# Kernel tuning notes

Measured on AMD Instinct MI355X. Metric: run time of the kernel, lower is better.

Reference implementation:

```python
import jax, jax.numpy as jnp
import numpy as np

B, S, H, D = 4, 2048, 12, 64
HID = H * D  # 768
EPS = 1e-5


def _layer_norm(h, w, b):
    mu = jnp.mean(h, axis=-1, keepdims=True)
    var = jnp.mean((h - mu) ** 2, axis=-1, keepdims=True)
    return w * (h - mu) / jnp.sqrt(var + EPS) + b


def setup_inputs() -> dict:
    key = jax.random.key(0)
    ks = jax.random.split(key, 12)
    sc = 1.0 / np.sqrt(HID)
    inp = {
        "x": jax.random.normal(ks[0], (B, S, HID), jnp.float32),
        "ln1_w": jnp.ones((HID,), jnp.float32),
        "ln1_b": jnp.zeros((HID,), jnp.float32),
        "Wq": jax.random.normal(ks[1], (HID, HID), jnp.float32) * sc,
        "bq": jnp.zeros((HID,), jnp.float32),
        "Wk": jax.random.normal(ks[2], (HID, HID), jnp.float32) * sc,
        "bk": jnp.zeros((HID,), jnp.float32),
        "Wv": jax.random.normal(ks[3], (HID, HID), jnp.float32) * sc,
        "bv": jnp.zeros((HID,), jnp.float32),
        "Wo": jax.random.normal(ks[4], (HID, HID), jnp.float32) * sc,
        "bo": jnp.zeros((HID,), jnp.float32),
        "ln2_w": jnp.ones((HID,), jnp.float32),
        "ln2_b": jnp.zeros((HID,), jnp.float32),
        "W1": jax.random.normal(ks[5], (HID, 4 * HID), jnp.float32) * sc,
        "b1": jnp.zeros((4 * HID,), jnp.float32),
        "W2": jax.random.normal(ks[6], (4 * HID, HID), jnp.float32) * (1.0 / np.sqrt(4 * HID)),
        "b2": jnp.zeros((HID,), jnp.float32),
    }
    return inp


def _split_heads(t):
    # (B, S, H*D) -> (B, H, S, D)
    b, s, _ = t.shape
    return t.reshape(b, s, H, -1).transpose(0, 2, 1, 3)


def _merge_heads(t):
    # (B, H, S, D) -> (B, S, H*D)
    b, h, s, d = t.shape
    return t.transpose(0, 2, 1, 3).reshape(b, s, h * d)


def _attention(h, Wq, bq, Wk, bk, Wv, bv, Wo, bo):
    q = _split_heads(h @ Wq + bq)  # (B,H,S,D)
    k = _split_heads(h @ Wk + bk)
    v = _split_heads(h @ Wv + bv)
    scores = jnp.einsum("bhqd,bhkd->bhqk", q, k) / jnp.sqrt(jnp.asarray(D, h.dtype))
    causal = jnp.tril(jnp.ones((q.shape[2], q.shape[2]), bool))  # (S,S)
    scores = jnp.where(causal, scores, jnp.finfo(scores.dtype).min)
    w = jax.nn.softmax(scores, axis=-1)
    out = jnp.einsum("bhqk,bhkd->bhqd", w, v)
    return _merge_heads(out) @ Wo + bo


def reference(x, ln1_w, ln1_b, Wq, bq, Wk, bk, Wv, bv, Wo, bo, ln2_w, ln2_b, W1, b1, W2, b2):
    # Pre-LN transformer block: x + attn(LN(x)); then x + MLP(LN(x))
    a = _attention(_layer_norm(x, ln1_w, ln1_b), Wq, bq, Wk, bk, Wv, bv, Wo, bo)
    x = x + a
    h = _layer_norm(x, ln2_w, ln2_b)
    m = jax.nn.gelu(h @ W1 + b1, approximate=False) @ W2 + b2
    return x + m
```

## Files before the change

kernel.cpp:

```cpp
#include <hip/hip_runtime.h>
#include <cmath>
#include <stdint.h>

typedef unsigned short u16;
typedef __attribute__((ext_vector_type(8))) short short8;
typedef __attribute__((ext_vector_type(4))) float f32x4;
typedef __attribute__((ext_vector_type(4))) unsigned int u32x4;

#define HID 768
#define FF  3072
#define SEQ 2048
#define NHEAD 12
#define NROWS 8192

__device__ __forceinline__ float bf2f(u16 u){ return __uint_as_float(((unsigned)u)<<16); }
__device__ __forceinline__ u16 f2bf(float f){
  unsigned x = __float_as_uint(f);
  x += 0x7fffu + ((x>>16)&1u);
  return (u16)(x>>16);
}
__device__ __forceinline__ unsigned pack2(float a, float b){
  return (unsigned)f2bf(a) | ((unsigned)f2bf(b) << 16);
}
__device__ __forceinline__ void gload16(const void* g, void* l){
  __builtin_amdgcn_global_load_lds((const __attribute__((address_space(1))) unsigned*)g,
                                   (__attribute__((address_space(3))) unsigned*)l, 16, 0, 0);
}

__global__ __launch_bounds__(256) void wconv(const float* __restrict__ in,
                                             u16* __restrict__ out, int K, int N)
{
  __shared__ float t[32][33];
  const int bk = blockIdx.x*32, bn = blockIdx.y*32;
  const int tn = threadIdx.x & 31, tk = threadIdx.x >> 5;
  #pragma unroll
  for (int j=0;j<4;++j)
    t[tk+8*j][tn] = in[(size_t)(bk+tk+8*j)*N + bn + tn];
  __syncthreads();
  #pragma unroll
  for (int j=0;j<4;++j)
    out[(size_t)(bn+tk+8*j)*K + bk + tn] = f2bf(t[tn][tk+8*j]);
}

__global__ __launch_bounds__(256) void tconv(const u16* __restrict__ in,
                                             u16* __restrict__ out, int K, int N)
{
  __shared__ u16 t[32][34];
  const int bk = blockIdx.x*32, bn = blockIdx.y*32;
  const int tn = threadIdx.x & 31, tk = threadIdx.x >> 5;
  #pragma unroll
  for (int j=0;j<4;++j)
    t[tk+8*j][tn] = in[(size_t)(bk+tk+8*j)*N + bn + tn];
  __syncthreads();
  #pragma unroll
  for (int j=0;j<4;++j)
    out[(size_t)(bn+tk+8*j)*K + bk + tn] = t[tn][tk+8*j];
}

__global__ __launch_bounds__(256) void ln_k(const float* __restrict__ in,
    const float* __restrict__ gw, const float* __restrict__ gb,
    u16* __restrict__ out)
{
  const int row = blockIdx.x*4 + (threadIdx.x>>6);
  const int l = threadIdx.x & 63;
  const float* p = in + (size_t)row*HID;
  float4 v[3];
  float s=0.f, ss=0.f;
  #pragma unroll
  for (int j=0;j<3;++j){
    v[j] = *(const float4*)(p + j*256 + l*4);
    s  += v[j].x + v[j].y + v[j].z + v[j].w;
    ss += v[j].x*v[j].x + v[j].y*v[j].y + v[j].z*v[j].z + v[j].w*v[j].w;
  }
  #pragma unroll
  for (int m=1;m<64;m<<=1){
    s  += __shfl_xor(s,  m, 64);
    ss += __shfl_xor(ss, m, 64);
  }
  const float mu = s * (1.f/768.f);
  const float rstd = rsqrtf(ss*(1.f/768.f) - mu*mu + 1e-5f);
  #pragma unroll
  for (int j=0;j<3;++j){
    const float4 wv = *(const float4*)(gw + j*256 + l*4);
    const float4 bv = *(const float4*)(gb + j*256 + l*4);
    ushort4 o;
    o.x = f2bf((v[j].x-mu)*rstd*wv.x + bv.x);
    o.y = f2bf((v[j].y-mu)*rstd*wv.y + bv.y);
    o.z = f2bf((v[j].z-mu)*rstd*wv.z + bv.z);
    o.w = f2bf((v[j].w-mu)*rstd*wv.w + bv.w);
    *(ushort4*)(out + (size_t)row*HID + j*256 + l*4) = o;
  }
}

template<int MODE>
__global__ __launch_bounds__(256) void gemm_bt(const u16* __restrict__ A,
    const u16* __restrict__ Bt, const float* __restrict__ bias0,
    const float* __restrict__ bias1, const float* __restrict__ bias2,
    const float* __restrict__ res, void* __restrict__ outp,
    int N, int K, long wstride, long ostride)
{
  __shared__ __align__(16) u16 sA[2][128*32];
  __shared__ __align__(16) u16 sB[2][128*32];
  const int tid = threadIdx.x, l = tid&63, w = tid>>6;
  const int wr = w>>1, wc = w&1, hi = l>>4, lo = l&15;
  const int bm = blockIdx.x*128, bn = blockIdx.y*128;
  const int z = blockIdx.z;
  const u16* Bz = Bt + (size_t)z * (size_t)wstride;
  const float* bias = (z==0) ? bias0 : ((z==1)? bias1 : bias2);

  const u16* Arow = A  + (size_t)bm*K;
  const u16* Brow = Bz + (size_t)bn*K;

  const f32x4 zv = {0.f,0.f,0.f,0.f};
  f32x4 acc[4][4];
  #pragma unroll
  for (int i=0;i<4;++i)
    #pragma unroll
    for (int j=0;j<4;++j) acc[i][j] = zv;

  const int r0_ = tid>>2, off_ = (tid&3)*8;
  const int r1_ = r0_ + 64;

  {
    gload16(Arow + (size_t)r0_*K + off_, (char*)sA[0] + tid*16);
    gload16(Brow + (size_t)r0_*K + off_, (char*)sB[0] + tid*16);
    gload16(Arow + (size_t)r1_*K + off_, (char*)sA[0] + (tid+256)*16);
    gload16(Brow + (size_t)r1_*K + off_, (char*)sB[0] + (tid+256)*16);
  }
  __syncthreads();

  const int NT = K >> 5;
  int cur = 0;
  for (int t=0; t<NT; ++t){
    if (t+1 < NT){
      const int kt = (t+1) << 5;
      gload16(Arow + (size_t)r0_*K + kt + off_, (char*)sA[cur^1] + tid*16);
      gload16(Brow + (size_t)r0_*K + kt + off_, (char*)sB[cur^1] + tid*16);
      gload16(Arow + (size_t)r1_*K + kt + off_, (char*)sA[cur^1] + (tid+256)*16);
      gload16(Brow + (size_t)r1_*K + kt + off_, (char*)sB[cur^1] + (tid+256)*16);
    }
    short8 af[4], bfv[4];
    #pragma unroll
    for (int i=0;i<4;++i){
      af[i]  = *(const short8*)(sA[cur] + (wr*64 + i*16 + lo)*32 + hi*8);
      bfv[i] = *(const short8*)(sB[cur] + (wc*64 + i*16 + lo)*32 + hi*8);
    }
    #pragma unroll
    for (int mi=0;mi<4;++mi)
      #pragma unroll
      for (int ni=0;ni<4;++ni)
        acc[mi][ni] = __builtin_amdgcn_mfma_f32_16x16x32_bf16(af[mi], bfv[ni], acc[mi][ni], 0,0,0);
    __syncthreads();
    cur ^= 1;
  }

  #pragma unroll
  for (int mi=0;mi<4;++mi)
    #pragma unroll
    for (int ni=0;ni<4;++ni){
      const int r0 = bm + wr*64 + mi*16 + 4*hi;
      const int cc = bn + wc*64 + ni*16 + lo;
      const float bv = bias[cc];
      #pragma unroll
      for (int g=0; g<4; ++g){
        const size_t idx = (size_t)(r0+g)*N + cc;
        float v = acc[mi][ni][g] + bv;
        if (MODE == 0){
          ((u16*)outp + (size_t)z*(size_t)ostride)[idx] = f2bf(v);
        } else if (MODE == 1){
          ((float*)outp)[idx] = res[idx] + v;
        } else {
          float u = v*(0.7978845608f + 0.0356774081f*v*v);
          float e = __expf(2.f*u);
          float th = 1.f - 2.f/(1.f + e);
          ((u16*)outp)[idx] = f2bf(0.5f*v*(1.f + th));
        }
      }
    }
}

__global__ __launch_bounds__(256, 4) void attn_k(const u16* __restrict__ Qm,
                                                 const u16* __restrict__ Km,
                                                 const u16* __restrict__ Vt,
                                                 u16* __restrict__ Om)
{
  __shared__ __align__(16) u16 sK [64*64];
  __shared__ __align__(16) u16 sVT[64*64];
  const int tid = threadIdx.x, l = tid & 63, w = tid >> 6;
  const int hi = l >> 4, lo = l & 15;
  const int idx = blockIdx.x;
  const int qb = 31 - (idx / 48);
  const int bh = idx % 48;
  const int b = bh / NHEAD, h = bh - (bh / NHEAD) * NHEAD;
  const size_t rb = (size_t)b * SEQ;
  const int qw = qb*64 + w*16;

  short8 qf[2];
  #pragma unroll
  for (int ks=0; ks<2; ++ks){
    short8 t = *(const short8*)(Qm + (rb + qw + lo)*HID + h*64 + ks*32 + hi*8);
    #pragma unroll
    for (int i=0;i<8;++i) t[i] = (short)f2bf(bf2f((u16)t[i]) * 0.125f);
    qf[ks] = t;
  }

  const f32x4 zv = {0.f,0.f,0.f,0.f};
  f32x4 oa[4] = {zv, zv, zv, zv};
  float m = -INFINITY, lsum = 0.f;
  const int srcA = (((2*hi)  & 3) << 4) | lo;
  const int srcB = (((2*hi+1)& 3) << 4) | lo;

  for (int t=0; t<=qb; ++t){
    const int kv0 = t*64;
    __syncthreads();
    #pragma unroll
    for (int j=0;j<2;++j){
      int c = tid + 256*j;
      int row = c >> 3;
      int d0 = ((c&7) ^ (row&7))*8;
      gload16(Km + (rb + kv0 + row)*HID + h*64 + d0, (char*)sK + c*16);
    }
    #pragma unroll
    for (int j=0;j<2;++j){
      int c = tid + 256*j;
      int row = c >> 3;
      int k0 = ((c&7) ^ (row&7))*8;
      gload16(Vt + (size_t)(h*64 + row)*NROWS + rb + kv0 + k0, (char*)sVT + c*16);
    }
    __syncthreads();

    f32x4 sc[4] = {zv, zv, zv, zv};
    #pragma unroll
    for (int ks=0;ks<2;++ks){
      #pragma unroll
      for (int ni=0;ni<4;++ni){
        short8 kf = *(const short8*)(sK + (ni*16 + lo)*64 + ((ks*32 + hi*8) ^ ((lo&7)*8)));
        sc[ni] = __builtin_amdgcn_mfma_f32_16x16x32_bf16(kf, qf[ks], sc[ni], 0,0,0);
      }
    }

    if (t == qb){
      #pragma unroll
      for (int ni=0;ni<4;++ni)
        #pragma unroll
        for (int g=0; g<4; ++g){
          int kg = kv0 + ni*16 + 4*hi + g;
          if (kg > qw + lo) sc[ni][g] = -INFINITY;
        }
    }

    float pm = sc[0][0];
    #pragma unroll
    for (int ni=0;ni<4;++ni)
      #pragma unroll
      for (int g=0; g<4; ++g) pm = fmaxf(pm, sc[ni][g]);
    pm = fmaxf(pm, __shfl_xor(pm, 16, 64));
    pm = fmaxf(pm, __shfl_xor(pm, 32, 64));
    const float mnew = fmaxf(m, pm);
    const float alpha = __expf(m - mnew);
    float ps = 0.f;
    #pragma unroll
    for (int ni=0;ni<4;++ni)
      #pragma unroll
      for (int g=0; g<4; ++g){
        float e = __expf(sc[ni][g] - mnew);
        sc[ni][g] = e;
        ps += e;
      }
    ps += __shfl_xor(ps, 16, 64);
    ps += __shfl_xor(ps, 32, 64);
    lsum = lsum*alpha + ps;
    m = mnew;
    #pragma unroll
    for (int nd=0;nd<4;++nd){
      oa[nd][0]*=alpha; oa[nd][1]*=alpha; oa[nd][2]*=alpha; oa[nd][3]*=alpha;
    }

    #pragma unroll
    for (int ks=0;ks<2;++ks){
      unsigned pkA0 = pack2(sc[2*ks  ][0], sc[2*ks  ][1]);
      unsigned pkA1 = pack2(sc[2*ks  ][2], sc[2*ks  ][3]);
      unsigned pkB0 = pack2(sc[2*ks+1][0], sc[2*ks+1][1]);
      unsigned pkB1 = pack2(sc[2*ks+1][2], sc[2*ks+1][3]);
      unsigned a0 = (unsigned)__shfl((int)pkA0, srcA, 64);
      unsigned b0 = (unsigned)__shfl((int)pkB0, srcA, 64);
      unsigned a1 = (unsigned)__shfl((int)pkA1, srcA, 64);
      unsigned b1 = (unsigned)__shfl((int)pkB1, srcA, 64);
      unsigned a2 = (unsigned)__shfl((int)pkA0, srcB, 64);
      unsigned b2 = (unsigned)__shfl((int)pkB0, srcB, 64);
      unsigned a3 = (unsigned)__shfl((int)pkA1, srcB, 64);
      unsigned b3 = (unsigned)__shfl((int)pkB1, srcB, 64);
      union { u32x4 u; short8 s; } pf;
      pf.u = (u32x4){ (hi<2)?a0:b0, (hi<2)?a1:b1, (hi<2)?a2:b2, (hi<2)?a3:b3 };

      #pragma unroll
      for (int nd=0;nd<4;++nd){
        short8 vf = *(const short8*)(sVT + (nd*16 + lo)*64 + ((ks*32 + hi*8) ^ ((lo&7)*8)));
        oa[nd] = __builtin_amdgcn_mfma_f32_16x16x32_bf16(vf, pf.s, oa[nd], 0,0,0);
      }
    }
  }

  const float inv = 1.f / lsum;
  #pragma unroll
  for (int nd=0;nd<4;++nd){
    ushort4 o;
    o.x = f2bf(oa[nd][0]*inv);
    o.y = f2bf(oa[nd][1]*inv);
    o.z = f2bf(oa[nd][2]*inv);
    o.w = f2bf(oa[nd][3]*inv);
    *(ushort4*)(Om + (rb + qw + lo)*HID + h*64 + nd*16 + 4*hi) = o;
  }
}

extern "C" void kernel_launch(void* const* d_in, const int* in_sizes, int n_in,
                              void* d_out, int out_size, void* d_ws, size_t ws_size,
                              hipStream_t stream)
{
  const float* x    = (const float*)d_in[0];
  const float* ln1w = (const float*)d_in[1];
  const float* ln1b = (const float*)d_in[2];
  const float* Wq   = (const float*)d_in[3];
  const float* bq   = (const float*)d_in[4];
  const float* Wk   = (const float*)d_in[5];
  const float* bk   = (const float*)d_in[6];
  const float* Wv   = (const float*)d_in[7];
  const float* bv   = (const float*)d_in[8];
  const float* Wo   = (const float*)d_in[9];
  const float* bo   = (const float*)d_in[10];
  const float* ln2w = (const float*)d_in[11];
  const float* ln2b = (const float*)d_in[12];
  const float* W1   = (const float*)d_in[13];
  const float* b1   = (const float*)d_in[14];
  const float* W2   = (const float*)d_in[15];
  const float* b2   = (const float*)d_in[16];

  u16* wq_t = (u16*)d_ws;
  u16* wk_t = wq_t + 589824;
  u16* wv_t = wk_t + 589824;
  u16* wo_t = wv_t + 589824;
  u16* w1_t = wo_t + 589824;
  u16* w2_t = w1_t + 2359296;
  u16* hbf  = w2_t + 2359296;
  u16* qb_  = hbf + 6291456;
  u16* kb_  = qb_ + 6291456;
  u16* vb_  = kb_ + 6291456;
  u16* atb  = vb_ + 6291456;
  u16* ub   = qb_;
  float* x2 = (float*)(atb + 6291456);

  const size_t need = 102236160ull;
  if (ws_size < need) return;

  dim3 blk(256);
  wconv<<<dim3(24,24), blk, 0, stream>>>(Wq, wq_t, 768, 768);
  wconv<<<dim3(24,24), blk, 0, stream>>>(Wk, wk_t, 768, 768);
  wconv<<<dim3(24,24), blk, 0, stream>>>(Wv, wv_t, 768, 768);
  wconv<<<dim3(24,24), blk, 0, stream>>>(Wo, wo_t, 768, 768);
  wconv<<<dim3(24,96), blk, 0, stream>>>(W1, w1_t, 768, 3072);
  wconv<<<dim3(96,24), blk, 0, stream>>>(W2, w2_t, 3072, 768);

  ln_k<<<2048, blk, 0, stream>>>(x, ln1w, ln1b, hbf);

  gemm_bt<0><<<dim3(64,6,3), blk, 0, stream>>>(hbf, wq_t, bq, bk, bv,
      nullptr, (void*)qb_, 768, 768, 589824L, 6291456L);
  tconv<<<dim3(256,24), blk, 0, stream>>>(vb_, hbf, 8192, 768);

  attn_k<<<dim3(1536), blk, 0, stream>>>(qb_, kb_, hbf, atb);

  gemm_bt<1><<<dim3(64,6,1), blk, 0, stream>>>(atb, wo_t, bo, bo, bo,
      x, (void*)x2, 768, 768, 0L, 0L);

  ln_k<<<2048, blk, 0, stream>>>(x2, ln2w, ln2b, hbf);

  gemm_bt<2><<<dim3(64,24,1), blk, 0, stream>>>(hbf, w1_t, b1, b1, b1,
      nullptr, (void*)ub, 3072, 768, 0L, 0L);

  gemm_bt<1><<<dim3(64,6,1), blk, 0, stream>>>(ub, w2_t, b2, b2, b2,
      x2, d_out, 768, 3072, 0L, 0L);
}
```

Baseline: 384.0 us.

## Narrow GEMM N-tiles, use exp2 softmax with lazy rescale and packed bf16 convert

The GEMM is templated on the N tile width. The QKV, out-projection and W2 GEMMs now use 64-wide tiles, doubling block count on the 768-wide outputs to fill more compute units. Attention folds log2(e) into the Q scale so it can use hardware exp2, and skips the rescaling of the accumulator and running sum unless the row max grows by more than 10. It also replaces manual bf16 rounding with the v_cvt_pk_bf16_f32 instruction. The tradeoffs are less data reuse per GEMM tile and slightly different rounding and overflow headroom in softmax.

Measured after the change: 397.4 us. +3.5%, slower.

```diff
diff --git a/kernel.cpp b/kernel.cpp
--- a/kernel.cpp
+++ b/kernel.cpp
@@ -19,8 +19,10 @@
   x += 0x7fffu + ((x>>16)&1u);
   return (u16)(x>>16);
 }
-__device__ __forceinline__ unsigned pack2(float a, float b){
-  return (unsigned)f2bf(a) | ((unsigned)f2bf(b) << 16);
+__device__ __forceinline__ unsigned cvtpk(float a, float b){
+  unsigned r;
+  asm("v_cvt_pk_bf16_f32 %0, %1, %2" : "=v"(r) : "v"(a), "v"(b));
+  return r;
 }
 __device__ __forceinline__ void gload16(const void* g, void* l){
   __builtin_amdgcn_global_load_lds((const __attribute__((address_space(1))) unsigned*)g,
@@ -92,18 +94,19 @@
   }
 }
 
-template<int MODE>
+template<int MODE, int BN>
 __global__ __launch_bounds__(256) void gemm_bt(const u16* __restrict__ A,
     const u16* __restrict__ Bt, const float* __restrict__ bias0,
     const float* __restrict__ bias1, const float* __restrict__ bias2,
     const float* __restrict__ res, void* __restrict__ outp,
     int N, int K, long wstride, long ostride)
 {
+  constexpr int NI = BN/32;
   __shared__ __align__(16) u16 sA[2][128*32];
-  __shared__ __align__(16) u16 sB[2][128*32];
+  __shared__ __align__(16) u16 sB[2][BN*32];
   const int tid = threadIdx.x, l = tid&63, w = tid>>6;
   const int wr = w>>1, wc = w&1, hi = l>>4, lo = l&15;
-  const int bm = blockIdx.x*128, bn = blockIdx.y*128;
+  const int bm = blockIdx.x*128, bn = blockIdx.y*BN;
   const int z = blockIdx.z;
   const u16* Bz = Bt + (size_t)z * (size_t)wstride;
   const float* bias = (z==0) ? bias0 : ((z==1)? bias1 : bias2);
@@ -112,21 +115,20 @@
   const u16* Brow = Bz + (size_t)bn*K;
 
   const f32x4 zv = {0.f,0.f,0.f,0.f};
-  f32x4 acc[4][4];
+  f32x4 acc[4][NI];
   #pragma unroll
   for (int i=0;i<4;++i)
     #pragma unroll
-    for (int j=0;j<4;++j) acc[i][j] = zv;
+    for (int j=0;j<NI;++j) acc[i][j] = zv;
 
   const int r0_ = tid>>2, off_ = (tid&3)*8;
   const int r1_ = r0_ + 64;
 
-  {
-    gload16(Arow + (size_t)r0_*K + off_, (char*)sA[0] + tid*16);
-    gload16(Brow + (size_t)r0_*K + off_, (char*)sB[0] + tid*16);
-    gload16(Arow + (size_t)r1_*K + off_, (char*)sA[0] + (tid+256)*16);
+  gload16(Arow + (size_t)r0_*K + off_, (char*)sA[0] + tid*16);
+  gload16(Arow + (size_t)r1_*K + off_, (char*)sA[0] + (tid+256)*16);
+  gload16(Brow + (size_t)r0_*K + off_, (char*)sB[0] + tid*16);
+  if constexpr (BN==128)
     gload16(Brow + (size_t)r1_*K + off_, (char*)sB[0] + (tid+256)*16);
-  }
   __syncthreads();
 
   const int NT = K >> 5;
@@ -135,20 +137,22 @@
     if (t+1 < NT){
       const int kt = (t+1) << 5;
       gload16(Arow + (size_t)r0_*K + kt + off_, (char*)sA[cur^1] + tid*16);
+      gload16(Arow + (size_t)r1_*K + kt + off_, (char*)sA[cur^1] + (tid+256)*16);
       gload16(Brow + (size_t)r0_*K + kt + off_, (char*)sB[cur^1] + tid*16);
-      gload16(Arow + (size_t)r1_*K + kt + off_, (char*)sA[cur^1] + (tid+256)*16);
-      gload16(Brow + (size_t)r1_*K + kt + off_, (char*)sB[cur^1] + (tid+256)*16);
-    }
-    short8 af[4], bfv[4];
-    #pragma unroll
-    for (int i=0;i<4;++i){
+      if constexpr (BN==128)
+        gload16(Brow + (size_t)r1_*K + kt + off_, (char*)sB[cur^1] + (tid+256)*16);
+    }
+    short8 af[4], bfv[NI];
+    #pragma unroll
+    for (int i=0;i<4;++i)
       af[i]  = *(const short8*)(sA[cur] + (wr*64 + i*16 + lo)*32 + hi*8);
-      bfv[i] = *(const short8*)(sB[cur] + (wc*64 + i*16 + lo)*32 + hi*8);
-    }
+    #pragma unroll
+    for (int i=0;i<NI;++i)
+      bfv[i] = *(const short8*)(sB[cur] + (wc*(BN/2) + i*16 + lo)*32 + hi*8);
     #pragma unroll
     for (int mi=0;mi<4;++mi)
       #pragma unroll
-      for (int ni=0;ni<4;++ni)
+      for (int ni=0;ni<NI;++ni)
         acc[mi][ni] = __builtin_amdgcn_mfma_f32_16x16x32_bf16(af[mi], bfv[ni], acc[mi][ni], 0,0,0);
     __syncthreads();
     cur ^= 1;
@@ -157,9 +161,9 @@
   #pragma unroll
   for (int mi=0;mi<4;++mi)
     #pragma unroll
-    for (int ni=0;ni<4;++ni){
+    for (int ni=0;ni<NI;++ni){
       const int r0 = bm + wr*64 + mi*16 + 4*hi;
-      const int cc = bn + wc*64 + ni*16 + lo;
+      const int cc = bn + wc*(BN/2) + ni*16 + lo;
       const float bv = bias[cc];
       #pragma unroll
       for (int g=0; g<4; ++g){
@@ -200,7 +204,7 @@
   for (int ks=0; ks<2; ++ks){
     short8 t = *(const short8*)(Qm + (rb + qw + lo)*HID + h*64 + ks*32 + hi*8);
     #pragma unroll
-    for (int i=0;i<8;++i) t[i] = (short)f2bf(bf2f((u16)t[i]) * 0.125f);
+    for (int i=0;i<8;++i) t[i] = (short)f2bf(bf2f((u16)t[i]) * 0.1803368801f);
     qf[ks] = t;
   }
 
@@ -249,49 +253,54 @@
         }
     }
 
-    float pm = sc[0][0];
-    #pragma unroll
-    for (int ni=0;ni<4;++ni)
-      #pragma unroll
-      for (int g=0; g<4; ++g) pm = fmaxf(pm, sc[ni][g]);
+    float a0 = fmaxf(fmaxf(sc[0][0], sc[0][1]), fmaxf(sc[0][2], sc[0][3]));
+    float a1 = fmaxf(fmaxf(sc[1][0], sc[1][1]), fmaxf(sc[1][2], sc[1][3]));
+    float a2 = fmaxf(fmaxf(sc[2][0], sc[2][1]), fmaxf(sc[2][2], sc[2][3]));
+    float a3 = fmaxf(fmaxf(sc[3][0], sc[3][1]), fmaxf(sc[3][2], sc[3][3]));
+    float pm = fmaxf(fmaxf(a0, a1), fmaxf(a2, a3));
     pm = fmaxf(pm, __shfl_xor(pm, 16, 64));
     pm = fmaxf(pm, __shfl_xor(pm, 32, 64));
-    const float mnew = fmaxf(m, pm);
-    const float alpha = __expf(m - mnew);
+
+    if (!__all(pm - m <= 10.f)){
+      const float mnew = fmaxf(m, pm);
+      const float alpha = __builtin_amdgcn_exp2f(m - mnew);
+      lsum *= alpha;
+      #pragma unroll
+      for (int nd=0;nd<4;++nd){
+        oa[nd][0]*=alpha; oa[nd][1]*=alpha; oa[nd][2]*=alpha; oa[nd][3]*=alpha;
+      }
+      m = mnew;
+    }
+
     float ps = 0.f;
     #pragma unroll
     for (int ni=0;ni<4;++ni)
       #pragma unroll
       for (int g=0; g<4; ++g){
-        float e = __expf(sc[ni][g] - mnew);
+        float e = __builtin_amdgcn_exp2f(sc[ni][g] - m);
         sc[ni][g] = e;
         ps += e;
       }
     ps += __shfl_xor(ps, 16, 64);
     ps += __shfl_xor(ps, 32, 64);
-    lsum = lsum*alpha + ps;
-    m = mnew;
-    #pragma unroll
-    for (int nd=0;nd<4;++nd){
-      oa[nd][0]*=alpha; oa[nd][1]*=alpha; oa[nd][2]*=alpha; oa[nd][3]*=alpha;
-    }
+    lsum += ps;
 
     #pragma unroll
     for (int ks=0;ks<2;++ks){
-      unsigned pkA0 = pack2(sc[2*ks  ][0], sc[2*ks  ][1]);
-      unsigned pkA1 = pack2(sc[2*ks  ][2], sc[2*ks  ][3]);
-      unsigned pkB0 = pack2(sc[2*ks+1][0], sc[2*ks+1][1]);
-      unsigned pkB1 = pack2(sc[2*ks+1][2], sc[2*ks+1][3]);
-      unsigned a0 = (unsigned)__shfl((int)pkA0, srcA, 64);
-      unsigned b0 = (unsigned)__shfl((int)pkB0, srcA, 64);
-      unsigned a1 = (unsigned)__shfl((int)pkA1, srcA, 64);
-      unsigned b1 = (unsigned)__shfl((int)pkB1, srcA, 64);
-      unsigned a2 = (unsigned)__shfl((int)pkA0, srcB, 64);
-      unsigned b2 = (unsigned)__shfl((int)pkB0, srcB, 64);
-      unsigned a3 = (unsigned)__shfl((int)pkA1, srcB, 64);
-      unsigned b3 = (unsigned)__shfl((int)pkB1, srcB, 64);
+      unsigned pkA0 = cvtpk(sc[2*ks  ][0], sc[2*ks  ][1]);
+      unsigned pkA1 = cvtpk(sc[2*ks  ][2], sc[2*ks  ][3]);
+      unsigned pkB0 = cvtpk(sc[2*ks+1][0], sc[2*ks+1][1]);
+      unsigned pkB1 = cvtpk(sc[2*ks+1][2], sc[2*ks+1][3]);
+      unsigned a0u = (unsigned)__shfl((int)pkA0, srcA, 64);
+      unsigned b0u = (unsigned)__shfl((int)pkB0, srcA, 64);
+      unsigned a1u = (unsigned)__shfl((int)pkA1, srcA, 64);
+      unsigned b1u = (unsigned)__shfl((int)pkB1, srcA, 64);
+      unsigned a2u = (unsigned)__shfl((int)pkA0, srcB, 64);
+      unsigned b2u = (unsigned)__shfl((int)pkB0, srcB, 64);
+      unsigned a3u = (unsigned)__shfl((int)pkA1, srcB, 64);
+      unsigned b3u = (unsigned)__shfl((int)pkB1, srcB, 64);
       union { u32x4 u; short8 s; } pf;
-      pf.u = (u32x4){ (hi<2)?a0:b0, (hi<2)?a1:b1, (hi<2)?a2:b2, (hi<2)?a3:b3 };
+      pf.u = (u32x4){ (hi<2)?a0u:b0u, (hi<2)?a1u:b1u, (hi<2)?a2u:b2u, (hi<2)?a3u:b3u };
 
       #pragma unroll
       for (int nd=0;nd<4;++nd){
@@ -362,20 +371,20 @@
 
   ln_k<<<2048, blk, 0, stream>>>(x, ln1w, ln1b, hbf);
 
-  gemm_bt<0><<<dim3(64,6,3), blk, 0, stream>>>(hbf, wq_t, bq, bk, bv,
+  gemm_bt<0,64><<<dim3(64,12,3), blk, 0, stream>>>(hbf, wq_t, bq, bk, bv,
       nullptr, (void*)qb_, 768, 768, 589824L, 6291456L);
   tconv<<<dim3(256,24), blk, 0, stream>>>(vb_, hbf, 8192, 768);
 
   attn_k<<<dim3(1536), blk, 0, stream>>>(qb_, kb_, hbf, atb);
 
-  gemm_bt<1><<<dim3(64,6,1), blk, 0, stream>>>(atb, wo_t, bo, bo, bo,
+  gemm_bt<1,64><<<dim3(64,12,1), blk, 0, stream>>>(atb, wo_t, bo, bo, bo,
       x, (void*)x2, 768, 768, 0L, 0L);
 
   ln_k<<<2048, blk, 0, stream>>>(x2, ln2w, ln2b, hbf);
 
-  gemm_bt<2><<<dim3(64,24,1), blk, 0, stream>>>(hbf, w1_t, b1, b1, b1,
+  gemm_bt<2,128><<<dim3(64,24,1), blk, 0, stream>>>(hbf, w1_t, b1, b1, b1,
       nullptr, (void*)ub, 3072, 768, 0L, 0L);
 
-  gemm_bt<1><<<dim3(64,6,1), blk, 0, stream>>>(ub, w2_t, b2, b2, b2,
+  gemm_bt<1,64><<<dim3(64,12,1), blk, 0, stream>>>(ub, w2_t, b2, b2, b2,
       x2, d_out, 768, 3072, 0L, 0L);
 }
```
